# Optimization experiments

Hardware: AMD Instinct MI355X
Metric: run time of the kernel (lower is better)

The kernel has to match this reference:

```python
import jax, jax.numpy as jnp
import numpy as np

CUTOFF = 10.0          # init: cutoff
K = 32                 # init: max_num_neighbors
BOX = 50.0             # spatial extent of the point cloud
N_GRAPHS = 8


def setup_inputs() -> dict:
    key = jax.random.key(0)
    k1, k2 = jax.random.split(key)
    N = 8192
    pos = jax.random.uniform(k1, (N, 3), dtype=jnp.float32) * BOX
    batch = jnp.sort(jax.random.randint(k2, (N,), 0, N_GRAPHS)).astype(jnp.int64)
    return {"pos": pos, "batch": batch}


def _radius_graph_edges(pos, batch):
    """Fixed-shape radius_graph: per node, up to K nearest same-batch neighbors
    within CUTOFF (no self), then self-loops appended. Padded edges masked."""
    N = pos.shape[0]
    # squared pairwise distances via gram trick: [N, N]
    x2 = jnp.sum(pos * pos, axis=-1)
    d2 = x2[:, None] + x2[None, :] - 2.0 * (pos @ pos.T)
    valid = (batch[:, None] == batch[None, :]) & (d2 <= CUTOFF * CUTOFF)
    valid = valid & ~jnp.eye(N, dtype=bool)  # loop=False in radius_graph
    score = jnp.where(valid, -d2, -jnp.inf)
    top_val, top_idx = jax.lax.top_k(score, K)   # nearest K neighbors per node
    valid_k = jnp.isfinite(top_val)              # [N, K]
    # edge (row=j neighbor source, col=i center target), flattened to N*K
    col = jnp.repeat(jnp.arange(N), K)
    row = top_idx.reshape(-1)
    mask = valid_k.reshape(-1)
    # append self-loops (add_self_loops)
    ar = jnp.arange(N)
    row = jnp.concatenate([row, ar])
    col = jnp.concatenate([col, ar])
    mask = jnp.concatenate([mask, jnp.ones((N,), dtype=bool)])
    row = jnp.where(mask, row, 0)  # safe index for padded edges
    return row.astype(jnp.int32), col.astype(jnp.int32), mask


def _edge_weight(pos, row, col, mask):
    diff = pos[row] - pos[col]              # [E, 3]
    sq = jnp.sum(diff * diff, axis=-1)
    # safe norm: zero (self-loop / padded) distances get weight 0, grad 0
    w = jnp.where(sq > 0, jnp.sqrt(jnp.where(sq > 0, sq, 1.0)), 0.0)
    return w * mask


def reference(pos, batch):
    row, col, mask = _radius_graph_edges(pos, batch)
    edge_index = jnp.stack([row, col])       # [2, N*K + N]
    edge_weight = _edge_weight(pos, row, col, mask)
    return edge_index, edge_weight, mask
```

## Files before the change

kernel.cpp:

```cpp
#include <hip/hip_runtime.h>


#define NPTS 8192
#define KNN 32
#define NG 8
#define MAXC 192
#define EDGES (NPTS * KNN + NPTS)

__device__ __forceinline__ float bfq(float f) {
    union { float f; unsigned int i; } v;
    v.f = f;
    unsigned int b = v.i;
    unsigned int r = (b + 0x7FFFu + ((b >> 16) & 1u)) & 0xFFFF0000u;
    v.i = r;
    return v.f;
}

__global__ __launch_bounds__(256) void radius_graph_kernel(
        const float* __restrict__ pos,
        const int*   __restrict__ batch32,
        float*       __restrict__ out) {
    const int i = blockIdx.x;
    __shared__ float s_d2[MAXC];
    __shared__ int   s_idx[MAXC];
    __shared__ int   s_cnt;
    __shared__ int   s_se[2];

    if (threadIdx.x == 0) s_cnt = 0;

    const int stride = (batch32[NPTS - 1] != NG - 1) ? 2 : 1;
    const int g = batch32[i * stride];

    if (threadIdx.x < 2) {
        const int v = g + (int)threadIdx.x;
        int lo = 0, hi = NPTS;
        while (lo < hi) {
            int mid = (lo + hi) >> 1;
            if (batch32[mid * stride] < v) lo = mid + 1; else hi = mid;
        }
        s_se[threadIdx.x] = lo;
    }

    const float xi = pos[3 * i + 0];
    const float yi = pos[3 * i + 1];
    const float zi = pos[3 * i + 2];
    const float x2i = __fadd_rn(__fadd_rn(__fmul_rn(xi, xi), __fmul_rn(yi, yi)),
                                __fmul_rn(zi, zi));
    __syncthreads();
    const int s = s_se[0];
    const int e = s_se[1];

    for (int j = s + threadIdx.x; j < e; j += blockDim.x) {
        if (j == i) continue;
        const float xj = pos[3 * j + 0];
        const float yj = pos[3 * j + 1];
        const float zj = pos[3 * j + 2];
        const float x2j = __fadd_rn(__fadd_rn(__fmul_rn(xj, xj), __fmul_rn(yj, yj)),
                                    __fmul_rn(zj, zj));
        float dot = __fmul_rn(xi, xj);
        dot = __fmaf_rn(yi, yj, dot);
        dot = __fmaf_rn(zi, zj, dot);
        const float d2 = __fsub_rn(__fadd_rn(x2i, x2j), __fmul_rn(2.0f, dot));
        if (d2 <= 100.0f) {
            int p = atomicAdd(&s_cnt, 1);
            if (p < MAXC) { s_d2[p] = d2; s_idx[p] = j; }
        }
    }
    __syncthreads();

    const int cnt = min(s_cnt, MAXC);
    const int c = (int)threadIdx.x;
    const int E = EDGES;
    const float fci = bfq((float)i);

    if (c < cnt) {
        const float dc = s_d2[c];
        const int   ic = s_idx[c];
        int rank = 0;
        for (int q = 0; q < cnt; ++q) {
            const float dq = s_d2[q];
            if (dq < dc || (dq == dc && s_idx[q] < ic)) rank++;
        }
        if (rank < KNN) {
            const int slot = i * KNN + rank;
            const float dx = __fsub_rn(pos[3 * ic + 0], xi);
            const float dy = __fsub_rn(pos[3 * ic + 1], yi);
            const float dz = __fsub_rn(pos[3 * ic + 2], zi);
            const float sq = __fadd_rn(__fadd_rn(__fmul_rn(dx, dx), __fmul_rn(dy, dy)),
                                       __fmul_rn(dz, dz));
            const float w = (sq > 0.0f) ? __fsqrt_rn(sq) : 0.0f;
            out[slot]         = bfq((float)ic);
            out[E + slot]     = fci;
            out[2 * E + slot] = bfq(w);
            out[3 * E + slot] = 1.0f;
        }
    }
    if (c < KNN && c >= cnt) {
        const int slot = i * KNN + c;
        out[slot]         = 0.0f;
        out[E + slot]     = fci;
        out[2 * E + slot] = 0.0f;
        out[3 * E + slot] = 0.0f;
    }
    if (c == 0) {
        const int slot = NPTS * KNN + i;
        out[slot]         = fci;
        out[E + slot]     = fci;
        out[2 * E + slot] = 0.0f;
        out[3 * E + slot] = 1.0f;
    }
}

extern "C" void kernel_launch(void* const* d_in, const int* in_sizes, int n_in,
                              void* d_out, int out_size, void* d_ws, size_t ws_size,
                              hipStream_t stream) {
    const float* pos   = (const float*)d_in[0];
    const int* batch32 = (const int*)d_in[1];
    float* out = (float*)d_out;

    radius_graph_kernel<<<NPTS, 256, 0, stream>>>(pos, batch32, out);
}
```

Baseline: 83.76 us.

## Assign one wavefront per point, compact candidates with ballot, precompute batch bounds

Each 256-thread block now processes four query points, one per 64-lane wavefront, instead of one point per block. Candidates within the cutoff are compacted with a ballot/popcount prefix instead of shared-memory atomics. Per-graph start/end offsets are computed once in a separate small kernel instead of a binary search in every block. The cost is an extra kernel launch. Each wavefront now scans roughly 1024 same-graph points serially in chunks of 64, so the per-wave loop is longer but there are far fewer blocks.

```diff
diff --git a/kernel.cpp b/kernel.cpp
--- a/kernel.cpp
+++ b/kernel.cpp
@@ -6,6 +6,8 @@
 #define NG 8
 #define MAXC 192
 #define EDGES (NPTS * KNN + NPTS)
+
+__device__ int g_bounds[NG + 1];
 
 __device__ __forceinline__ float bfq(float f) {
     union { float f; unsigned int i; } v;
@@ -16,78 +18,94 @@
     return v.f;
 }
 
+__device__ __forceinline__ int batch_stride(const int* __restrict__ b) {
+    return (b[NPTS - 1] != NG - 1) ? 2 : 1;
+}
+
+__global__ __launch_bounds__(256) void bounds_kernel(
+        const int* __restrict__ batch32) {
+    const int tid = blockIdx.x * 256 + threadIdx.x;
+    if (tid >= NPTS) return;
+    const int stride = batch_stride(batch32);
+    const int g  = batch32[tid * stride];
+    const int gp = (tid == 0) ? -1 : batch32[(tid - 1) * stride];
+    for (int v = gp + 1; v <= g; ++v) g_bounds[v] = tid;
+    if (tid == NPTS - 1) {
+        for (int v = g + 1; v <= NG; ++v) g_bounds[v] = NPTS;
+    }
+}
+
 __global__ __launch_bounds__(256) void radius_graph_kernel(
         const float* __restrict__ pos,
         const int*   __restrict__ batch32,
         float*       __restrict__ out) {
-    const int i = blockIdx.x;
-    __shared__ float s_d2[MAXC];
-    __shared__ int   s_idx[MAXC];
-    __shared__ int   s_cnt;
-    __shared__ int   s_se[2];
+    const int wave = threadIdx.x >> 6;
+    const int lane = threadIdx.x & 63;
+    const int i = (blockIdx.x << 2) + wave;
 
-    if (threadIdx.x == 0) s_cnt = 0;
+    __shared__ float2 s_cand[4][MAXC];
 
-    const int stride = (batch32[NPTS - 1] != NG - 1) ? 2 : 1;
+    const int stride = batch_stride(batch32);
     const int g = batch32[i * stride];
-
-    if (threadIdx.x < 2) {
-        const int v = g + (int)threadIdx.x;
-        int lo = 0, hi = NPTS;
-        while (lo < hi) {
-            int mid = (lo + hi) >> 1;
-            if (batch32[mid * stride] < v) lo = mid + 1; else hi = mid;
-        }
-        s_se[threadIdx.x] = lo;
-    }
+    const int s = g_bounds[g];
+    const int e = g_bounds[g + 1];
 
     const float xi = pos[3 * i + 0];
     const float yi = pos[3 * i + 1];
     const float zi = pos[3 * i + 2];
     const float x2i = __fadd_rn(__fadd_rn(__fmul_rn(xi, xi), __fmul_rn(yi, yi)),
                                 __fmul_rn(zi, zi));
-    __syncthreads();
-    const int s = s_se[0];
-    const int e = s_se[1];
 
-    for (int j = s + threadIdx.x; j < e; j += blockDim.x) {
-        if (j == i) continue;
-        const float xj = pos[3 * j + 0];
-        const float yj = pos[3 * j + 1];
-        const float zj = pos[3 * j + 2];
-        const float x2j = __fadd_rn(__fadd_rn(__fmul_rn(xj, xj), __fmul_rn(yj, yj)),
-                                    __fmul_rn(zj, zj));
-        float dot = __fmul_rn(xi, xj);
-        dot = __fmaf_rn(yi, yj, dot);
-        dot = __fmaf_rn(zi, zj, dot);
-        const float d2 = __fsub_rn(__fadd_rn(x2i, x2j), __fmul_rn(2.0f, dot));
-        if (d2 <= 100.0f) {
-            int p = atomicAdd(&s_cnt, 1);
-            if (p < MAXC) { s_d2[p] = d2; s_idx[p] = j; }
+    int cnt = 0;
+    for (int j0 = s; j0 < e; j0 += 64) {
+        const int j = j0 + lane;
+        bool ok = false;
+        float d2 = 0.0f;
+        if (j < e && j != i) {
+            const float xj = pos[3 * j + 0];
+            const float yj = pos[3 * j + 1];
+            const float zj = pos[3 * j + 2];
+            const float x2j = __fadd_rn(
+                __fadd_rn(__fmul_rn(xj, xj), __fmul_rn(yj, yj)),
+                __fmul_rn(zj, zj));
+            float dot = __fmul_rn(xi, xj);
+            dot = __fmaf_rn(yi, yj, dot);
+            dot = __fmaf_rn(zi, zj, dot);
+            d2 = __fsub_rn(__fadd_rn(x2i, x2j), __fmul_rn(2.0f, dot));
+            ok = (d2 <= 100.0f);
         }
+        const unsigned long long m = __ballot(ok);
+        if (ok) {
+            const int p = cnt + __popcll(m & ((1ull << lane) - 1ull));
+            if (p < MAXC) s_cand[wave][p] = make_float2(d2, __int_as_float(j));
+        }
+        cnt += (int)__popcll(m);
     }
+    cnt = min(cnt, MAXC);
     __syncthreads();
 
-    const int cnt = min(s_cnt, MAXC);
-    const int c = (int)threadIdx.x;
     const int E = EDGES;
     const float fci = bfq((float)i);
+    const int ne = min(cnt, KNN);
 
-    if (c < cnt) {
-        const float dc = s_d2[c];
-        const int   ic = s_idx[c];
+    for (int c = lane; c < cnt; c += 64) {
+        const float2 pc = s_cand[wave][c];
+        const float dc = pc.x;
+        const int   ic = __float_as_int(pc.y);
         int rank = 0;
         for (int q = 0; q < cnt; ++q) {
-            const float dq = s_d2[q];
-            if (dq < dc || (dq == dc && s_idx[q] < ic)) rank++;
+            const float2 pq = s_cand[wave][q];
+            const float dq = pq.x;
+            if (dq < dc || (dq == dc && __float_as_int(pq.y) < ic)) rank++;
         }
         if (rank < KNN) {
             const int slot = i * KNN + rank;
             const float dx = __fsub_rn(pos[3 * ic + 0], xi);
             const float dy = __fsub_rn(pos[3 * ic + 1], yi);
             const float dz = __fsub_rn(pos[3 * ic + 2], zi);
-            const float sq = __fadd_rn(__fadd_rn(__fmul_rn(dx, dx), __fmul_rn(dy, dy)),
-                                       __fmul_rn(dz, dz));
+            const float sq = __fadd_rn(
+                __fadd_rn(__fmul_rn(dx, dx), __fmul_rn(dy, dy)),
+                __fmul_rn(dz, dz));
             const float w = (sq > 0.0f) ? __fsqrt_rn(sq) : 0.0f;
             out[slot]         = bfq((float)ic);
             out[E + slot]     = fci;
@@ -95,14 +113,14 @@
             out[3 * E + slot] = 1.0f;
         }
     }
-    if (c < KNN && c >= cnt) {
+    for (int c = ne + lane; c < KNN; c += 64) {
         const int slot = i * KNN + c;
         out[slot]         = 0.0f;
         out[E + slot]     = fci;
         out[2 * E + slot] = 0.0f;
         out[3 * E + slot] = 0.0f;
     }
-    if (c == 0) {
+    if (lane == 0) {
         const int slot = NPTS * KNN + i;
         out[slot]         = fci;
         out[E + slot]     = fci;
@@ -118,5 +136,6 @@
     const int* batch32 = (const int*)d_in[1];
     float* out = (float*)d_out;
 
-    radius_graph_kernel<<<NPTS, 256, 0, stream>>>(pos, batch32, out);
+    bounds_kernel<<<32, 256, 0, stream>>>(batch32);
+    radius_graph_kernel<<<2048, 256, 0, stream>>>(pos, batch32, out);
 }
```

New measurement: 72.86 us. 1.15x faster.
